# Optimization experiments

Hardware: AMD Instinct MI355X
Metric: run time of the kernel (lower is better)

## Reference

```python
import jax, jax.numpy as jnp
import numpy as np
from jax import lax

PAD_IDX = 0  # padding_index from init
B, T, E, H, V = 128, 24, 512, 512, 10000


def setup_inputs() -> dict:
    key = jax.random.key(0)
    ks = jax.random.split(key, 10)
    return {
        "images": jax.random.normal(ks[0], (B, H), jnp.float32),
        "captions": jax.random.randint(ks[1], (B, T), 0, V),
        "captions_length": jax.random.randint(ks[2], (B,), 1, T + 1),
        "W_emb": jax.random.normal(ks[3], (V, E), jnp.float32) * 0.02,
        "W_ih": jax.random.normal(ks[4], (4 * H, E), jnp.float32) * 0.02,
        "W_hh": jax.random.normal(ks[5], (4 * H, H), jnp.float32) * 0.02,
        "b_ih": jax.random.normal(ks[6], (4 * H,), jnp.float32) * 0.02,
        "b_hh": jax.random.normal(ks[7], (4 * H,), jnp.float32) * 0.02,
        "W_out": jax.random.normal(ks[8], (V, H), jnp.float32) * 0.02,
        "b_out": jax.random.normal(ks[9], (V,), jnp.float32) * 0.02,
    }


def reference(images, captions, captions_length, W_emb, W_ih, W_hh, b_ih, b_hh, W_out, b_out):
    # embedding with padding_idx: padding row forced to zero
    emb_table = W_emb.at[PAD_IDX].set(0.0)
    x = emb_table[captions]  # [B, T, E]
    bdim = images.shape[0]
    hdim = W_hh.shape[1]
    vocab = W_out.shape[0]
    bias = b_ih + b_hh

    def step(carry, xt):
        h, c = carry
        # PyTorch LSTMCell gate order: i, f, g, o
        gates = xt @ W_ih.T + h @ W_hh.T + bias  # [B, 4H]
        i, f, g, o = jnp.split(gates, 4, axis=-1)
        c = jax.nn.sigmoid(f) * c + jax.nn.sigmoid(i) * jnp.tanh(g)
        h = jax.nn.sigmoid(o) * jnp.tanh(c)
        logits = h @ W_out.T + b_out  # [B, V]
        return (h, c), logits

    c0 = jnp.zeros((bdim, hdim), images.dtype)
    _, ys = lax.scan(step, (images, c0), jnp.transpose(x, (1, 0, 2)))  # ys: [T, B, V]

    # deterministic <SOS>-like start output: one-hot at index 1, prepended at t=0
    start = jnp.zeros((vocab,), images.dtype).at[1].set(1.0)
    outputs = jnp.concatenate(
        [jnp.broadcast_to(start, (bdim, 1, vocab)), jnp.transpose(ys, (1, 0, 2))], axis=1
    )  # [B, T+1, V]
    return outputs, captions_length - 1
```

## Files before the change

kernel.cpp:

```cpp
#include <hip/hip_runtime.h>

constexpr int B_  = 128;
constexpr int T_  = 24;
constexpr int E_  = 512;
constexpr int H_  = 512;
constexpr int V_  = 10000;
constexpr int G4  = 2048;
constexpr int TP1 = 25;
constexpr int VP  = 10112;

typedef __attribute__((ext_vector_type(8))) short bf16x8;
typedef __attribute__((ext_vector_type(4))) short short4v;
typedef __attribute__((ext_vector_type(4))) float f32x4;

#define MFMA_16x16x32_BF16(a, b, c) __builtin_amdgcn_mfma_f32_16x16x32_bf16((a), (b), (c), 0, 0, 0)

__device__ inline unsigned short f2bf(float f) {
    unsigned int u = __float_as_uint(f);
    unsigned int r = (u + 0x7FFFu + ((u >> 16) & 1u)) >> 16;
    return (unsigned short)r;
}

__device__ inline void gl16(const unsigned short* g, unsigned short* l) {
    __builtin_amdgcn_global_load_lds(
        (const __attribute__((address_space(1))) unsigned int*)g,
        (__attribute__((address_space(3))) unsigned int*)l, 16, 0, 0);
}

__device__ inline int swz16(int row, int lq) {
    return (((row << 2) | lq) ^ (row & 7)) << 3;
}

__global__ __launch_bounds__(256) void k_cvt_all(const float* __restrict__ Wih,
                                                 const float* __restrict__ Whh,
                                                 const float* __restrict__ Wout,
                                                 const float* __restrict__ images,
                                                 unsigned short* __restrict__ dWih,
                                                 unsigned short* __restrict__ dWhh,
                                                 unsigned short* __restrict__ dWout,
                                                 unsigned short* __restrict__ dimg) {
    int b = blockIdx.x;
    const float* src; unsigned short* dst; int i;
    if (b < 1024)      { src = Wih;    dst = dWih;  i = b * 256 + threadIdx.x; }
    else if (b < 2048) { src = Whh;    dst = dWhh;  i = (b - 1024) * 256 + threadIdx.x; }
    else if (b < 7048) { src = Wout;   dst = dWout; i = (b - 2048) * 256 + threadIdx.x; }
    else               { src = images; dst = dimg;  i = (b - 7048) * 256 + threadIdx.x; }
    float4 v = ((const float4*)src)[i];
    short4v o;
    o[0] = (short)f2bf(v.x); o[1] = (short)f2bf(v.y);
    o[2] = (short)f2bf(v.z); o[3] = (short)f2bf(v.w);
    ((short4v*)dst)[i] = o;
}

__global__ __launch_bounds__(256) void k_embed(const float* __restrict__ Wemb,
                                               const int* __restrict__ captions,
                                               unsigned short* __restrict__ Xemb) {
    int i = blockIdx.x * 256 + threadIdx.x;
    if (i >= 3072 * 128) return;
    int row = i >> 7;
    int k4  = i & 127;
    int b = row & 127, t = row >> 7;
    int tok = captions[b * T_ + t];
    short4v o = {0, 0, 0, 0};
    if (tok > 0 && tok < V_) {
        float4 v = ((const float4*)(Wemb + (long)tok * E_))[k4];
        o[0] = (short)f2bf(v.x); o[1] = (short)f2bf(v.y);
        o[2] = (short)f2bf(v.z); o[3] = (short)f2bf(v.w);
    }
    ((short4v*)Xemb)[(long)row * 128 + k4] = o;
}

__global__ __launch_bounds__(256) void k_start(float* __restrict__ out,
                                               const int* __restrict__ cap_len) {
    int idx = blockIdx.x * 256 + threadIdx.x;
    constexpr int Q = V_ / 4;
    if (idx < B_ * Q) {
        int b = idx / Q;
        int q = idx - b * Q;
        float4 zero = {0.f, 0.f, 0.f, 0.f};
        float4 one1 = {0.f, 1.f, 0.f, 0.f};
        ((float4*)out)[(long)b * (TP1 * Q) + q] = (q == 0) ? one1 : zero;
    }
    if (idx < B_) {
        out[(size_t)B_ * TP1 * V_ + idx] = (float)(cap_len[idx] - 1);
    }
}

__global__ __launch_bounds__(256) void k_pregemm(const unsigned short* __restrict__ Xemb,
                                                 const unsigned short* __restrict__ Wih,
                                                 const float* __restrict__ bih,
                                                 const float* __restrict__ bhh,
                                                 float* __restrict__ P) {
    __shared__ unsigned short ldsA[2][4096];
    __shared__ unsigned short ldsB[2][4096];
    int bid = blockIdx.x;
    int xcd = bid & 7;
    int q   = bid >> 3;
    int MI  = xcd * 3 + (q % 3);
    int NI  = q / 3;
    int i    = threadIdx.x;
    int w = i >> 6, lane = i & 63;
    int lm = lane & 15, lq = lane >> 4;
    int wr = w >> 1, wc = w & 1;

    int mm0 = ((i >> 2) & 7) ^ ((i >> 4) & 1);
    int li  = i ^ mm0;
    const unsigned short* gA = Xemb + (size_t)(MI * 128 + (li >> 2)) * 512 + (li & 3) * 8;
    const unsigned short* gB = Wih  + (size_t)(NI * 128 + (li >> 2)) * 512 + (li & 3) * 8;
    unsigned short* lA = &ldsA[0][0] + i * 8;
    unsigned short* lB = &ldsB[0][0] + i * 8;

    auto stage = [&](int buf, int ks) {
        int go = ks * 32;
        gl16(gA + go,            lA + buf * 4096);
        gl16(gA + go + 64 * 512, lA + buf * 4096 + 2048);
        gl16(gB + go,            lB + buf * 4096);
        gl16(gB + go + 64 * 512, lB + buf * 4096 + 2048);
    };

    f32x4 acc[4][4] = {};
    stage(0, 0);
    for (int ksi = 0; ksi < 16; ksi++) {
        int cur = ksi & 1;
        if (ksi < 15) stage(cur ^ 1, ksi + 1);
        __syncthreads();
        bf16x8 af[4], bfr[4];
        #pragma unroll
        for (int mi = 0; mi < 4; mi++)
            af[mi] = *(const bf16x8*)&ldsA[cur][swz16(wr * 64 + mi * 16 + lm, lq)];
        #pragma unroll
        for (int ni = 0; ni < 4; ni++)
            bfr[ni] = *(const bf16x8*)&ldsB[cur][swz16(wc * 64 + ni * 16 + lm, lq)];
        #pragma unroll
        for (int mi = 0; mi < 4; mi++)
            #pragma unroll
            for (int ni = 0; ni < 4; ni++)
                acc[mi][ni] = MFMA_16x16x32_BF16(af[mi], bfr[ni], acc[mi][ni]);
        __syncthreads();
    }

    float bias[4];
    #pragma unroll
    for (int ni = 0; ni < 4; ni++) {
        int n = NI * 128 + wc * 64 + ni * 16 + lm;
        bias[ni] = bih[n] + bhh[n];
    }
    #pragma unroll
    for (int mi = 0; mi < 4; mi++) {
        #pragma unroll
        for (int r = 0; r < 4; r++) {
            int m = MI * 128 + wr * 64 + mi * 16 + lq * 4 + r;
            #pragma unroll
            for (int ni = 0; ni < 4; ni++) {
                int n = NI * 128 + wc * 64 + ni * 16 + lm;
                P[(size_t)m * G4 + n] = acc[mi][ni][r] + bias[ni];
            }
        }
    }
}

__global__ __launch_bounds__(512) void k_step(const float* __restrict__ Pt,
                                              const unsigned short* __restrict__ h_in,
                                              const unsigned short* __restrict__ Whh,
                                              float* __restrict__ c,
                                              unsigned short* __restrict__ h_out,
                                              unsigned short* __restrict__ Hall_t,
                                              int t) {
    __shared__ float part[16][8][64];
    int w    = threadIdx.x >> 6;
    int lane = threadIdx.x & 63;
    int lm = lane & 15, lq = lane >> 4;
    int MI = blockIdx.x >> 5;
    int HG = blockIdx.x & 31;
    int hcol = HG * 16 + lm;
    int ks = w * 64;
    int brow = MI * 16 + lq * 4 + w;

    float pv0 = 0.f, pv1 = 0.f, pv2 = 0.f, pv3 = 0.f, cp = 0.f;
    if (w < 4) {
        const float* Pr = Pt + (size_t)brow * G4;
        pv0 = Pr[0 * 512 + hcol];
        pv1 = Pr[1 * 512 + hcol];
        pv2 = Pr[2 * 512 + hcol];
        pv3 = Pr[3 * 512 + hcol];
        if (t != 0) cp = c[brow * H_ + hcol];
    }

    const short* A  = (const short*)h_in + (long)(MI * 16 + lm) * H_ + ks;
    const short* B0 = (const short*)Whh + (long)(0 * 512 + hcol) * H_ + ks;
    const short* B1 = (const short*)Whh + (long)(1 * 512 + hcol) * H_ + ks;
    const short* B2 = (const short*)Whh + (long)(2 * 512 + hcol) * H_ + ks;
    const short* B3 = (const short*)Whh + (long)(3 * 512 + hcol) * H_ + ks;

    f32x4 acc[4] = {};
    #pragma unroll
    for (int kk = 0; kk < 2; kk++) {
        int ko = kk * 32 + lq * 8;
        bf16x8 a = *(const bf16x8*)(A + ko);
        acc[0] = MFMA_16x16x32_BF16(a, *(const bf16x8*)(B0 + ko), acc[0]);
        acc[1] = MFMA_16x16x32_BF16(a, *(const bf16x8*)(B1 + ko), acc[1]);
        acc[2] = MFMA_16x16x32_BF16(a, *(const bf16x8*)(B2 + ko), acc[2]);
        acc[3] = MFMA_16x16x32_BF16(a, *(const bf16x8*)(B3 + ko), acc[3]);
    }

    #pragma unroll
    for (int g = 0; g < 4; g++)
        #pragma unroll
        for (int r = 0; r < 4; r++)
            part[g * 4 + r][w][lane] = acc[g][r];
    __syncthreads();

    if (w < 4) {
        float gi = pv0, gf = pv1, gg = pv2, go = pv3;
        #pragma unroll
        for (int wp = 0; wp < 8; wp++) gi += part[0 * 4 + w][wp][lane];
        #pragma unroll
        for (int wp = 0; wp < 8; wp++) gf += part[1 * 4 + w][wp][lane];
        #pragma unroll
        for (int wp = 0; wp < 8; wp++) gg += part[2 * 4 + w][wp][lane];
        #pragma unroll
        for (int wp = 0; wp < 8; wp++) go += part[3 * 4 + w][wp][lane];
        float si = 1.f / (1.f + expf(-gi));
        float sf = 1.f / (1.f + expf(-gf));
        float so = 1.f / (1.f + expf(-go));
        float cn = sf * cp + si * tanhf(gg);
        float hn = so * tanhf(cn);
        c[brow * H_ + hcol] = cn;
        unsigned short hb = f2bf(hn);
        h_out[brow * H_ + hcol] = hb;
        Hall_t[brow * H_ + hcol] = hb;
    }
}

__global__ __launch_bounds__(256) void k_logits(const unsigned short* __restrict__ Hall,
                                                const unsigned short* __restrict__ Wout,
                                                const float* __restrict__ bout,
                                                float* __restrict__ out) {
    __shared__ unsigned short ldsA[2][4096];
    __shared__ unsigned short ldsB[2][4096];
    int bid = blockIdx.x;
    int xcd = bid & 7;
    int q   = bid >> 3;
    int MI  = xcd * 3 + (q % 3);
    int NI  = q / 3;
    int i    = threadIdx.x;
    int w = i >> 6, lane = i & 63;
    int lm = lane & 15, lq = lane >> 4;
    int wr = w >> 1, wc = w & 1;

    int mm0 = ((i >> 2) & 7) ^ ((i >> 4) & 1);
    int li  = i ^ mm0;
    const unsigned short* gA = Hall + (size_t)(MI * 128 + (li >> 2)) * 512 + (li & 3) * 8;
    const unsigned short* gB = Wout + (size_t)(NI * 128 + (li >> 2)) * 512 + (li & 3) * 8;
    unsigned short* lA = &ldsA[0][0] + i * 8;
    unsigned short* lB = &ldsB[0][0] + i * 8;

    auto stage = [&](int buf, int ks) {
        int go = ks * 32;
        gl16(gA + go,            lA + buf * 4096);
        gl16(gA + go + 64 * 512, lA + buf * 4096 + 2048);
        gl16(gB + go,            lB + buf * 4096);
        gl16(gB + go + 64 * 512, lB + buf * 4096 + 2048);
    };

    f32x4 acc[4][4] = {};
    stage(0, 0);
    for (int ksi = 0; ksi < 16; ksi++) {
        int cur = ksi & 1;
        if (ksi < 15) stage(cur ^ 1, ksi + 1);
        __syncthreads();
        bf16x8 af[4], bfr[4];
        #pragma unroll
        for (int mi = 0; mi < 4; mi++)
            af[mi] = *(const bf16x8*)&ldsA[cur][swz16(wr * 64 + mi * 16 + lm, lq)];
        #pragma unroll
        for (int ni = 0; ni < 4; ni++)
            bfr[ni] = *(const bf16x8*)&ldsB[cur][swz16(wc * 64 + ni * 16 + lm, lq)];
        #pragma unroll
        for (int mi = 0; mi < 4; mi++)
            #pragma unroll
            for (int ni = 0; ni < 4; ni++)
                acc[mi][ni] = MFMA_16x16x32_BF16(af[mi], bfr[ni], acc[mi][ni]);
        __syncthreads();
    }

    #pragma unroll
    for (int mi = 0; mi < 4; mi++) {
        #pragma unroll
        for (int r = 0; r < 4; r++) {
            int b = wr * 64 + mi * 16 + lq * 4 + r;
            float* orow = out + ((size_t)b * TP1 + MI + 1) * V_;
            #pragma unroll
            for (int ni = 0; ni < 4; ni++) {
                int n = NI * 128 + wc * 64 + ni * 16 + lm;
                if (n < V_) orow[n] = acc[mi][ni][r] + bout[n];
            }
        }
    }
}

extern "C" void kernel_launch(void* const* d_in, const int* in_sizes, int n_in,
                              void* d_out, int out_size, void* d_ws, size_t ws_size,
                              hipStream_t stream) {
    const float* images   = (const float*)d_in[0];
    const int*   captions = (const int*)d_in[1];
    const int*   cap_len  = (const int*)d_in[2];
    const float* Wemb     = (const float*)d_in[3];
    const float* Wih      = (const float*)d_in[4];
    const float* Whh      = (const float*)d_in[5];
    const float* bih      = (const float*)d_in[6];
    const float* bhh      = (const float*)d_in[7];
    const float* Wout     = (const float*)d_in[8];
    const float* bout     = (const float*)d_in[9];
    float* out = (float*)d_out;

    char* ws = (char*)d_ws;
    unsigned short* Wih_bf  = (unsigned short*)(ws);
    unsigned short* Whh_bf  = (unsigned short*)(ws + 2097152);
    unsigned short* Wout_bf = (unsigned short*)(ws + 4194304);
    unsigned short* Xemb    = (unsigned short*)(ws + 14548992);
    unsigned short* Hall    = (unsigned short*)(ws + 17694720);
    unsigned short* h0      = (unsigned short*)(ws + 20840448);
    unsigned short* h1      = (unsigned short*)(ws + 20971520);
    float*          cbuf    = (float*)(ws + 21102592);
    constexpr size_t P_OFF   = 21364736;
    constexpr size_t WS_NEED = P_OFF + 25165824;
    float* P = (ws_size >= WS_NEED) ? (float*)(ws + P_OFF) : (float*)d_out;

    k_cvt_all<<<7112, 256, 0, stream>>>(Wih, Whh, Wout, images,
                                        Wih_bf, Whh_bf, Wout_bf, h0);
    k_embed<<<1536, 256, 0, stream>>>(Wemb, captions, Xemb);

    k_pregemm<<<384, 256, 0, stream>>>(Xemb, Wih_bf, bih, bhh, P);

    for (int t = 0; t < T_; t++) {
        const unsigned short* hin  = (t & 1) ? h1 : h0;
        unsigned short*       hout = (t & 1) ? h0 : h1;
        k_step<<<256, 512, 0, stream>>>(P + (long)t * B_ * G4, hin, Whh_bf,
                                        cbuf, hout, Hall + (long)t * B_ * H_, t);
    }

    k_start<<<1250, 256, 0, stream>>>(out, cap_len);

    k_logits<<<1896, 256, 0, stream>>>(Hall, Wout_bf, bout, out);
}
```

Baseline: 376.7 us.

## Fuse LSTM timesteps into one persistent kernel with a global atomic barrier

Replaces the 24 per-timestep k_step launches with a single persistent k_lstm kernel of 256 blocks. Each block keeps its W_hh slice in registers across all steps and keeps the cell state in registers instead of global memory. Hidden state moves between blocks through agent-scope atomic loads and stores, and steps are separated by a grid-wide spin barrier on a counter that k_cvt_all resets. This removes per-step launch overhead and repeated weight reloads. In exchange it assumes all 256 blocks are co-resident, and correctness depends on relaxed atomics plus the barrier giving visibility.

```diff
diff --git a/kernel.cpp b/kernel.cpp
--- a/kernel.cpp
+++ b/kernel.cpp
@@ -7,7 +7,6 @@
 constexpr int V_  = 10000;
 constexpr int G4  = 2048;
 constexpr int TP1 = 25;
-constexpr int VP  = 10112;
 
 typedef __attribute__((ext_vector_type(8))) short bf16x8;
 typedef __attribute__((ext_vector_type(4))) short short4v;
@@ -38,8 +37,10 @@
                                                  unsigned short* __restrict__ dWih,
                                                  unsigned short* __restrict__ dWhh,
                                                  unsigned short* __restrict__ dWout,
-                                                 unsigned short* __restrict__ dimg) {
+                                                 unsigned short* __restrict__ dimg,
+                                                 unsigned* __restrict__ bar) {
     int b = blockIdx.x;
+    if (b == 0 && threadIdx.x == 0) { bar[0] = 0u; bar[1] = 0u; }
     const float* src; unsigned short* dst; int i;
     if (b < 1024)      { src = Wih;    dst = dWih;  i = b * 256 + threadIdx.x; }
     else if (b < 2048) { src = Whh;    dst = dWhh;  i = (b - 1024) * 256 + threadIdx.x; }
@@ -159,76 +160,111 @@
     }
 }
 
-__global__ __launch_bounds__(512) void k_step(const float* __restrict__ Pt,
-                                              const unsigned short* __restrict__ h_in,
-                                              const unsigned short* __restrict__ Whh,
-                                              float* __restrict__ c,
-                                              unsigned short* __restrict__ h_out,
-                                              unsigned short* __restrict__ Hall_t,
-                                              int t) {
-    __shared__ float part[16][8][64];
+__global__ __launch_bounds__(256, 1) void k_lstm(const float* __restrict__ P,
+                                                 const unsigned short* __restrict__ h0,
+                                                 unsigned* __restrict__ hx0,
+                                                 unsigned* __restrict__ hx1,
+                                                 unsigned short* __restrict__ Hall,
+                                                 const unsigned short* __restrict__ Whh,
+                                                 unsigned* __restrict__ bar) {
+    __shared__ float part[16][4][64];
     int w    = threadIdx.x >> 6;
     int lane = threadIdx.x & 63;
     int lm = lane & 15, lq = lane >> 4;
     int MI = blockIdx.x >> 5;
     int HG = blockIdx.x & 31;
     int hcol = HG * 16 + lm;
-    int ks = w * 64;
+    int ks = w * 128;
     int brow = MI * 16 + lq * 4 + w;
 
-    float pv0 = 0.f, pv1 = 0.f, pv2 = 0.f, pv3 = 0.f, cp = 0.f;
-    if (w < 4) {
-        const float* Pr = Pt + (size_t)brow * G4;
-        pv0 = Pr[0 * 512 + hcol];
-        pv1 = Pr[1 * 512 + hcol];
-        pv2 = Pr[2 * 512 + hcol];
-        pv3 = Pr[3 * 512 + hcol];
-        if (t != 0) cp = c[brow * H_ + hcol];
-    }
-
-    const short* A  = (const short*)h_in + (long)(MI * 16 + lm) * H_ + ks;
-    const short* B0 = (const short*)Whh + (long)(0 * 512 + hcol) * H_ + ks;
-    const short* B1 = (const short*)Whh + (long)(1 * 512 + hcol) * H_ + ks;
-    const short* B2 = (const short*)Whh + (long)(2 * 512 + hcol) * H_ + ks;
-    const short* B3 = (const short*)Whh + (long)(3 * 512 + hcol) * H_ + ks;
-
-    f32x4 acc[4] = {};
-    #pragma unroll
-    for (int kk = 0; kk < 2; kk++) {
-        int ko = kk * 32 + lq * 8;
-        bf16x8 a = *(const bf16x8*)(A + ko);
-        acc[0] = MFMA_16x16x32_BF16(a, *(const bf16x8*)(B0 + ko), acc[0]);
-        acc[1] = MFMA_16x16x32_BF16(a, *(const bf16x8*)(B1 + ko), acc[1]);
-        acc[2] = MFMA_16x16x32_BF16(a, *(const bf16x8*)(B2 + ko), acc[2]);
-        acc[3] = MFMA_16x16x32_BF16(a, *(const bf16x8*)(B3 + ko), acc[3]);
-    }
-
+    bf16x8 bw[4][4];
     #pragma unroll
     for (int g = 0; g < 4; g++)
         #pragma unroll
-        for (int r = 0; r < 4; r++)
-            part[g * 4 + r][w][lane] = acc[g][r];
-    __syncthreads();
-
-    if (w < 4) {
-        float gi = pv0, gf = pv1, gg = pv2, go = pv3;
-        #pragma unroll
-        for (int wp = 0; wp < 8; wp++) gi += part[0 * 4 + w][wp][lane];
-        #pragma unroll
-        for (int wp = 0; wp < 8; wp++) gf += part[1 * 4 + w][wp][lane];
-        #pragma unroll
-        for (int wp = 0; wp < 8; wp++) gg += part[2 * 4 + w][wp][lane];
-        #pragma unroll
-        for (int wp = 0; wp < 8; wp++) go += part[3 * 4 + w][wp][lane];
+        for (int kk = 0; kk < 4; kk++)
+            bw[g][kk] = *(const bf16x8*)((const short*)Whh +
+                          (size_t)(g * 512 + hcol) * 512 + ks + kk * 32 + lq * 8);
+
+    float cp = 0.f;
+
+    for (int t = 0; t < T_; t++) {
+        bf16x8 a[4];
+        if (t == 0) {
+            const unsigned short* A = h0 + (size_t)(MI * 16 + lm) * 512 + ks;
+            #pragma unroll
+            for (int kk = 0; kk < 4; kk++)
+                a[kk] = *(const bf16x8*)(A + kk * 32 + lq * 8);
+        } else {
+            const unsigned* HX = (t & 1) ? hx1 : hx0;
+            const unsigned* A = HX + ((size_t)(MI * 16 + lm) * 512 + ks) / 2;
+            #pragma unroll
+            for (int kk = 0; kk < 4; kk++) {
+                union { unsigned u[4]; bf16x8 v; } cv;
+                #pragma unroll
+                for (int j = 0; j < 4; j++)
+                    cv.u[j] = __hip_atomic_load(A + kk * 16 + lq * 4 + j,
+                                                __ATOMIC_RELAXED, __HIP_MEMORY_SCOPE_AGENT);
+                a[kk] = cv.v;
+            }
+        }
+
+        const float* Pr = P + (size_t)t * B_ * G4 + (size_t)brow * G4;
+        float pv0 = Pr[0 * 512 + hcol];
+        float pv1 = Pr[1 * 512 + hcol];
+        float pv2 = Pr[2 * 512 + hcol];
+        float pv3 = Pr[3 * 512 + hcol];
+
+        f32x4 acc[4] = {};
+        #pragma unroll
+        for (int kk = 0; kk < 4; kk++) {
+            acc[0] = MFMA_16x16x32_BF16(a[kk], bw[0][kk], acc[0]);
+            acc[1] = MFMA_16x16x32_BF16(a[kk], bw[1][kk], acc[1]);
+            acc[2] = MFMA_16x16x32_BF16(a[kk], bw[2][kk], acc[2]);
+            acc[3] = MFMA_16x16x32_BF16(a[kk], bw[3][kk], acc[3]);
+        }
+
+        #pragma unroll
+        for (int g = 0; g < 4; g++)
+            #pragma unroll
+            for (int r = 0; r < 4; r++)
+                part[g * 4 + r][w][lane] = acc[g][r];
+        __syncthreads();
+
+        float gi = part[0*4+w][0][lane] + part[0*4+w][1][lane] + part[0*4+w][2][lane] + part[0*4+w][3][lane] + pv0;
+        float gf = part[1*4+w][0][lane] + part[1*4+w][1][lane] + part[1*4+w][2][lane] + part[1*4+w][3][lane] + pv1;
+        float gg = part[2*4+w][0][lane] + part[2*4+w][1][lane] + part[2*4+w][2][lane] + part[2*4+w][3][lane] + pv2;
+        float go = part[3*4+w][0][lane] + part[3*4+w][1][lane] + part[3*4+w][2][lane] + part[3*4+w][3][lane] + pv3;
         float si = 1.f / (1.f + expf(-gi));
         float sf = 1.f / (1.f + expf(-gf));
         float so = 1.f / (1.f + expf(-go));
         float cn = sf * cp + si * tanhf(gg);
         float hn = so * tanhf(cn);
-        c[brow * H_ + hcol] = cn;
+        cp = cn;
         unsigned short hb = f2bf(hn);
-        h_out[brow * H_ + hcol] = hb;
-        Hall_t[brow * H_ + hcol] = hb;
+        Hall[(size_t)t * (B_ * H_) + brow * 512 + hcol] = hb;
+
+        if (t < T_ - 1) {
+            unsigned up = ((unsigned)(unsigned short)__shfl_down((int)hb, 1) << 16) | (unsigned)hb;
+            unsigned* HW = (t & 1) ? hx0 : hx1;
+            if (!(lm & 1))
+                __hip_atomic_store(HW + (brow * 512 + hcol) / 2, up,
+                                   __ATOMIC_RELAXED, __HIP_MEMORY_SCOPE_AGENT);
+            asm volatile("s_waitcnt vmcnt(0)" ::: "memory");
+            __syncthreads();
+            if (threadIdx.x == 0) {
+                unsigned prev = __hip_atomic_fetch_add(&bar[0], 1u, __ATOMIC_RELAXED,
+                                                       __HIP_MEMORY_SCOPE_AGENT);
+                if (prev == (unsigned)(t * 256 + 255)) {
+                    __hip_atomic_store(&bar[1], (unsigned)(t + 1), __ATOMIC_RELAXED,
+                                       __HIP_MEMORY_SCOPE_AGENT);
+                } else {
+                    while (__hip_atomic_load(&bar[1], __ATOMIC_RELAXED,
+                                             __HIP_MEMORY_SCOPE_AGENT) < (unsigned)(t + 1))
+                        __builtin_amdgcn_s_sleep(8);
+                }
+            }
+            __syncthreads();
+        }
     }
 }
 
@@ -321,24 +357,20 @@
     unsigned short* Xemb    = (unsigned short*)(ws + 14548992);
     unsigned short* Hall    = (unsigned short*)(ws + 17694720);
     unsigned short* h0      = (unsigned short*)(ws + 20840448);
-    unsigned short* h1      = (unsigned short*)(ws + 20971520);
-    float*          cbuf    = (float*)(ws + 21102592);
-    constexpr size_t P_OFF   = 21364736;
+    unsigned*       hx0     = (unsigned*)(ws + 20971520);
+    unsigned*       hx1     = (unsigned*)(ws + 21102592);
+    unsigned*       bar     = (unsigned*)(ws + 21233664);
+    constexpr size_t P_OFF   = 21233920;
     constexpr size_t WS_NEED = P_OFF + 25165824;
     float* P = (ws_size >= WS_NEED) ? (float*)(ws + P_OFF) : (float*)d_out;
 
     k_cvt_all<<<7112, 256, 0, stream>>>(Wih, Whh, Wout, images,
-                                        Wih_bf, Whh_bf, Wout_bf, h0);
+                                        Wih_bf, Whh_bf, Wout_bf, h0, bar);
     k_embed<<<1536, 256, 0, stream>>>(Wemb, captions, Xemb);
 
     k_pregemm<<<384, 256, 0, stream>>>(Xemb, Wih_bf, bih, bhh, P);
 
-    for (int t = 0; t < T_; t++) {
-        const unsigned short* hin  = (t & 1) ? h1 : h0;
-        unsigned short*       hout = (t & 1) ? h0 : h1;
-        k_step<<<256, 512, 0, stream>>>(P + (long)t * B_ * G4, hin, Whh_bf,
-                                        cbuf, hout, Hall + (long)t * B_ * H_, t);
-    }
+    k_lstm<<<256, 256, 0, stream>>>(P, h0, hx0, hx1, Hall, Whh_bf, bar);
 
     k_start<<<1250, 256, 0, stream>>>(out, cap_len);
 
```

Result: slower. 428.6 us (+13.8%).
